# Performance work log

Measured on AMD Instinct MI355X. Metric: run time of the kernel, lower is better.

The kernel has to match this reference:

```python
import jax, jax.numpy as jnp
import numpy as np

KERNEL_SIZE = 3
ITERATIONS = 4


def _box_conv(x, kernel):
    # x: [B,1,H,W], kernel: [1,1,k,k]; SAME padding via pad=(k-1)//2
    p = (KERNEL_SIZE - 1) // 2
    return jax.lax.conv_general_dilated(
        x, kernel,
        window_strides=(1, 1),
        padding=((p, p), (p, p)),
        dimension_numbers=("NCHW", "OIHW", "NCHW"),
    )


def setup_inputs() -> dict:
    key = jax.random.key(0)
    inputs = jax.random.uniform(key, (32, 1, 512, 512), dtype=jnp.float32)
    return {"inputs": inputs}


def reference(inputs) -> jnp.ndarray:
    # fixed box-filter kernel: every tap = 1/k^2, bias = 0 (frozen in torch module)
    kernel = jnp.full((1, 1, KERNEL_SIZE, KERNEL_SIZE), 1.0 / KERNEL_SIZE**2, dtype=inputs.dtype)
    blob = inputs
    for _ in range(ITERATIONS):
        # NOTE: original module convolves `inputs` (not previous blob) each iteration
        blob = _box_conv(inputs, kernel)
        blob = jax.nn.sigmoid((blob - 0.01) * 1000.0)
        blob = _box_conv(blob, kernel)
        blob = jax.nn.sigmoid((blob - 0.9) * 1000.0)
    return blob
```

## Files before the change

### kernel.cpp

```cpp
#include <hip/hip_runtime.h>


#define IMG 512
#define BH  8
#define NROWS (BH + 4)
#define NIT   (BH + 2)

__device__ __forceinline__ float steep_sig(float sum9, float bias) {
    float x = fmaf(sum9, 1000.0f / 9.0f, bias);
    return __builtin_amdgcn_rcpf(1.0f + __expf(-x));
}

__device__ __forceinline__ float4 f4add3(float4 a, float4 b, float4 c) {
    return make_float4(a.x + b.x + c.x, a.y + b.y + c.y,
                       a.z + b.z + c.z, a.w + b.w + c.w);
}

__global__ __launch_bounds__(256) void blobber_fused(const float* __restrict__ in,
                                                     float* __restrict__ out) {
    const int tid  = threadIdx.x;
    const int lane = tid & 63;
    const int gw   = blockIdx.x * 4 + (tid >> 6);
    const int band = gw & 63;
    const int img  = gw >> 6;
    const int y0   = band * BH;

    const int colL = 4 * lane;
    const int colR = 256 + 4 * lane;

    const float* ip = in  + (size_t)img * (IMG * IMG);
    float*       op = out + (size_t)img * (IMG * IMG);

    float4 inL[NROWS], inR[NROWS];
    #pragma unroll
    for (int k = 0; k < NROWS; ++k) {
        const int r = y0 - 2 + k;
        inL[k] = make_float4(0.f, 0.f, 0.f, 0.f);
        inR[k] = make_float4(0.f, 0.f, 0.f, 0.f);
        if ((unsigned)r < IMG) {
            inL[k] = *(const float4*)(ip + r * IMG + colL);
            inR[k] = *(const float4*)(ip + r * IMG + colR);
        }
    }

    const float4 z4 = make_float4(0.f, 0.f, 0.f, 0.f);
    float4 h2mL = z4, h2cL = z4, h2mR = z4, h2cR = z4;

    #pragma unroll
    for (int s = 0; s < NIT; ++s) {
        const int r = y0 - 1 + s;

        float4 vL = f4add3(inL[s], inL[s + 1], inL[s + 2]);
        float4 vR = f4add3(inR[s], inR[s + 1], inR[s + 2]);

        float Llft = __shfl_up(vL.w, 1);
        float Lrgt = __shfl_down(vL.x, 1);
        float Rlft = __shfl_up(vR.w, 1);
        float Rrgt = __shfl_down(vR.x, 1);
        float c256 = __shfl(vR.x, 0);
        float c255 = __shfl(vL.w, 63);
        if (lane == 0)  { Llft = 0.0f;  Rlft = c255; }
        if (lane == 63) { Lrgt = c256;  Rrgt = 0.0f; }

        float4 s1L, s1R;
        if ((unsigned)r < IMG) {
            s1L.x = steep_sig(Llft + vL.x + vL.y, -10.0f);
            s1L.y = steep_sig(vL.x + vL.y + vL.z, -10.0f);
            s1L.z = steep_sig(vL.y + vL.z + vL.w, -10.0f);
            s1L.w = steep_sig(vL.z + vL.w + Lrgt, -10.0f);
            s1R.x = steep_sig(Rlft + vR.x + vR.y, -10.0f);
            s1R.y = steep_sig(vR.x + vR.y + vR.z, -10.0f);
            s1R.z = steep_sig(vR.y + vR.z + vR.w, -10.0f);
            s1R.w = steep_sig(vR.z + vR.w + Rrgt, -10.0f);
        } else {
            s1L = z4; s1R = z4;
        }

        float sLl = __shfl_up(s1L.w, 1);
        float sLr = __shfl_down(s1L.x, 1);
        float sRl = __shfl_up(s1R.w, 1);
        float sRr = __shfl_down(s1R.x, 1);
        float s256 = __shfl(s1R.x, 0);
        float s255 = __shfl(s1L.w, 63);
        if (lane == 0)  { sLl = 0.0f;  sRl = s255; }
        if (lane == 63) { sLr = s256;  sRr = 0.0f; }

        float4 h2pL, h2pR;
        h2pL.x = sLl   + s1L.x + s1L.y;
        h2pL.y = s1L.x + s1L.y + s1L.z;
        h2pL.z = s1L.y + s1L.z + s1L.w;
        h2pL.w = s1L.z + s1L.w + sLr;
        h2pR.x = sRl   + s1R.x + s1R.y;
        h2pR.y = s1R.x + s1R.y + s1R.z;
        h2pR.z = s1R.y + s1R.z + s1R.w;
        h2pR.w = s1R.z + s1R.w + sRr;

        if (s >= 2) {
            const int oy = r - 1;
            float4 oL, oR;
            oL.x = steep_sig(h2mL.x + h2cL.x + h2pL.x, -900.0f);
            oL.y = steep_sig(h2mL.y + h2cL.y + h2pL.y, -900.0f);
            oL.z = steep_sig(h2mL.z + h2cL.z + h2pL.z, -900.0f);
            oL.w = steep_sig(h2mL.w + h2cL.w + h2pL.w, -900.0f);
            oR.x = steep_sig(h2mR.x + h2cR.x + h2pR.x, -900.0f);
            oR.y = steep_sig(h2mR.y + h2cR.y + h2pR.y, -900.0f);
            oR.z = steep_sig(h2mR.z + h2cR.z + h2pR.z, -900.0f);
            oR.w = steep_sig(h2mR.w + h2cR.w + h2pR.w, -900.0f);
            *(float4*)(op + oy * IMG + colL) = oL;
            *(float4*)(op + oy * IMG + colR) = oR;
        }

        h2mL = h2cL; h2cL = h2pL;
        h2mR = h2cR; h2cR = h2pR;
    }
}

extern "C" void kernel_launch(void* const* d_in, const int* in_sizes, int n_in,
                              void* d_out, int out_size, void* d_ws, size_t ws_size,
                              hipStream_t stream) {
    const float* in  = (const float*)d_in[0];
    float*       out = (float*)d_out;
    blobber_fused<<<dim3(512), dim3(256), 0, stream>>>(in, out);
}
```

Before: 84.63 us.

## Halve row band height and stream input rows through a rolling register window

Each wave now processes 4 output rows instead of 8, which doubles the grid to 1024 blocks for more parallelism and latency hiding. The input rows are no longer preloaded into a 12-row register array. A 3-row sliding window loads the next row inside the loop, which cuts register use and overlaps loads with compute. In exchange the halo overhead grows: 8 input rows are read and 6 stage-1 rows computed per 4 outputs, against 12 and 10 per 8 before.

Measured after the change: 84.18 us. Within noise of the previous version (-0.5%).

```diff
diff --git a/kernel.cpp b/kernel.cpp
--- a/kernel.cpp
+++ b/kernel.cpp
@@ -2,9 +2,8 @@
 
 
 #define IMG 512
-#define BH  8
-#define NROWS (BH + 4)
-#define NIT   (BH + 2)
+#define BH  4
+#define NIT (BH + 2)
 
 __device__ __forceinline__ float steep_sig(float sum9, float bias) {
     float x = fmaf(sum9, 1000.0f / 9.0f, bias);
@@ -21,8 +20,8 @@
     const int tid  = threadIdx.x;
     const int lane = tid & 63;
     const int gw   = blockIdx.x * 4 + (tid >> 6);
-    const int band = gw & 63;
-    const int img  = gw >> 6;
+    const int band = gw & 127;
+    const int img  = gw >> 7;
     const int y0   = band * BH;
 
     const int colL = 4 * lane;
@@ -31,27 +30,37 @@
     const float* ip = in  + (size_t)img * (IMG * IMG);
     float*       op = out + (size_t)img * (IMG * IMG);
 
-    float4 inL[NROWS], inR[NROWS];
-    #pragma unroll
-    for (int k = 0; k < NROWS; ++k) {
-        const int r = y0 - 2 + k;
-        inL[k] = make_float4(0.f, 0.f, 0.f, 0.f);
-        inR[k] = make_float4(0.f, 0.f, 0.f, 0.f);
-        if ((unsigned)r < IMG) {
-            inL[k] = *(const float4*)(ip + r * IMG + colL);
-            inR[k] = *(const float4*)(ip + r * IMG + colR);
-        }
+    const float4 z4 = make_float4(0.f, 0.f, 0.f, 0.f);
+
+    float4 aL = z4, bL = z4, cL = z4, aR = z4, bR = z4, cR = z4;
+    if (y0 - 2 >= 0) {
+        aL = *(const float4*)(ip + (y0 - 2) * IMG + colL);
+        aR = *(const float4*)(ip + (y0 - 2) * IMG + colR);
     }
+    if (y0 - 1 >= 0) {
+        bL = *(const float4*)(ip + (y0 - 1) * IMG + colL);
+        bR = *(const float4*)(ip + (y0 - 1) * IMG + colR);
+    }
+    cL = *(const float4*)(ip + y0 * IMG + colL);
+    cR = *(const float4*)(ip + y0 * IMG + colR);
 
-    const float4 z4 = make_float4(0.f, 0.f, 0.f, 0.f);
     float4 h2mL = z4, h2cL = z4, h2mR = z4, h2cR = z4;
 
     #pragma unroll
     for (int s = 0; s < NIT; ++s) {
         const int r = y0 - 1 + s;
 
-        float4 vL = f4add3(inL[s], inL[s + 1], inL[s + 2]);
-        float4 vR = f4add3(inR[s], inR[s + 1], inR[s + 2]);
+        float4 nL = z4, nR = z4;
+        if (s < NIT - 1) {
+            const int pr = r + 2;
+            if (pr < IMG) {
+                nL = *(const float4*)(ip + pr * IMG + colL);
+                nR = *(const float4*)(ip + pr * IMG + colR);
+            }
+        }
+
+        float4 vL = f4add3(aL, bL, cL);
+        float4 vR = f4add3(aR, bR, cR);
 
         float Llft = __shfl_up(vL.w, 1);
         float Lrgt = __shfl_down(vL.x, 1);
@@ -112,6 +121,9 @@
 
         h2mL = h2cL; h2cL = h2pL;
         h2mR = h2cR; h2cR = h2pR;
+
+        aL = bL; bL = cL; cL = nL;
+        aR = bR; bR = cR; cR = nR;
     }
 }
 
@@ -120,5 +132,5 @@
                               hipStream_t stream) {
     const float* in  = (const float*)d_in[0];
     float*       out = (float*)d_out;
-    blobber_fused<<<dim3(512), dim3(256), 0, stream>>>(in, out);
+    blobber_fused<<<dim3(1024), dim3(256), 0, stream>>>(in, out);
 }
```
